# Kernel tuning notes

Measured on AMD Instinct MI355X. Metric: run time of the kernel, lower is better.

The kernel has to match this reference:

```python
import jax, jax.numpy as jnp
import numpy as np

NUM_HEADS = 8
D_MODEL = 512
D_K = D_MODEL // NUM_HEADS


def setup_inputs() -> dict:
    key = jax.random.key(0)
    ks = jax.random.split(key, 16)
    B, L, Dq = 4, 2048, 512
    s = 1.0 / np.sqrt(D_MODEL)
    inp = {
        "query": jax.random.normal(ks[0], (B, L, Dq), jnp.float32),
        "key": jax.random.normal(ks[1], (B, L, Dq), jnp.float32),
        "value": jax.random.normal(ks[2], (B, L, Dq), jnp.float32),
        "mask": jax.random.randint(ks[3], (B, L), 0, 2, jnp.int32),
        "Wq": jax.random.normal(ks[4], (Dq, D_MODEL), jnp.float32) * s,
        "bq": jax.random.normal(ks[5], (D_MODEL,), jnp.float32) * s,
        "Wk": jax.random.normal(ks[6], (Dq, D_MODEL), jnp.float32) * s,
        "bk": jax.random.normal(ks[7], (D_MODEL,), jnp.float32) * s,
        "Wv": jax.random.normal(ks[8], (Dq, D_MODEL), jnp.float32) * s,
        "bv": jax.random.normal(ks[9], (D_MODEL,), jnp.float32) * s,
        "Wo": jax.random.normal(ks[10], (D_MODEL, D_MODEL), jnp.float32) * s,
        "bo": jax.random.normal(ks[11], (D_MODEL,), jnp.float32) * s,
    }
    return inp


def _mha(query, key, value, mask, Wq, bq, Wk, bk, Wv, bv, Wo, bo):
    B, Q, _ = query.shape
    KV = key.shape[1]
    # projections, split into heads: (B, H, L, d_k)
    q = (query @ Wq + bq).reshape(B, Q, NUM_HEADS, D_K).transpose(0, 2, 1, 3)
    k = (key @ Wk + bk).reshape(B, KV, NUM_HEADS, D_K).transpose(0, 2, 1, 3)
    v = (value @ Wv + bv).reshape(B, KV, NUM_HEADS, D_K).transpose(0, 2, 1, 3)
    # full (B, H, Q, KV) score matrix, as in the original module
    scores = jnp.einsum("bhqd,bhkd->bhqk", q, k) / jnp.sqrt(jnp.asarray(D_K, q.dtype))
    m = (mask == 0)[:, None, None, :]  # (B,1,1,KV) broadcasting like unsqueeze(1)
    min_val = jnp.finfo(scores.dtype).min
    scores = jnp.where(m, min_val, scores)
    attn = jax.nn.softmax(scores, axis=-1)
    attn = jnp.where(m, 0.0, attn)
    xs = jnp.einsum("bhqk,bhkd->bhqd", attn, v)
    xs = xs.transpose(0, 2, 1, 3).reshape(B, Q, NUM_HEADS * D_K)
    return xs @ Wo + bo


def reference(query, key, value, mask, Wq, bq, Wk, bk, Wv, bv, Wo, bo):
    return _mha(query, key, value, mask, Wq, bq, Wk, bk, Wv, bv, Wo, bo)
```

## Files before the change

### kernel.cpp

```cpp
#include <hip/hip_runtime.h>
#include <math.h>

#define Bq 4
#define Lq 2048
#define NH 8
#define LDP6 36

typedef __attribute__((ext_vector_type(8))) __bf16 bf16x8;
typedef __attribute__((ext_vector_type(4))) float f32x4;
#define MFMA16(a,b,c) __builtin_amdgcn_mfma_f32_16x16x32_bf16(a,b,c,0,0,0)

__device__ __forceinline__ void async16(const void* g, void* l) {
    __builtin_amdgcn_global_load_lds(
        (const __attribute__((address_space(1))) unsigned int*)g,
        (__attribute__((address_space(3))) unsigned int*)l, 16, 0, 0);
}

__device__ __forceinline__ void splitbf(float x, ushort& h, ushort& l) {
    unsigned u = __float_as_uint(x);
    h = (ushort)(u >> 16);
    float hf = __uint_as_float(u & 0xffff0000u);
    l = (ushort)(__float_as_uint(x - hf) >> 16);
}
__device__ __forceinline__ ushort rnebf(float x) {
    unsigned u = __float_as_uint(x);
    return (ushort)((u + 0x7fffu + ((u >> 16) & 1u)) >> 16);
}

__global__ __launch_bounds__(256) void prep_kernel(
    const float* __restrict__ W0, const float* __restrict__ W1,
    const float* __restrict__ W2, const float* __restrict__ W3,
    ushort* __restrict__ WTh, ushort* __restrict__ WTl,
    const int* __restrict__ mask, int* __restrict__ idx, int* __restrict__ nvalid,
    const float* __restrict__ X0, const float* __restrict__ X1, const float* __restrict__ X2,
    ushort* __restrict__ Xr)
{
    const int tid = threadIdx.x;
    const int z = blockIdx.z;
    if (z < 3) {
        const float* X = (z == 0) ? X0 : (z == 1) ? X1 : X2;
        const size_t ebase = (size_t)blockIdx.x * 2048 + (size_t)tid * 8;
        float4 a = *(const float4*)(X + ebase);
        float4 bb = *(const float4*)(X + ebase + 4);
        float vv[8] = {a.x, a.y, a.z, a.w, bb.x, bb.y, bb.z, bb.w};
        ushort hs[8];
        #pragma unroll
        for (int j = 0; j < 8; ++j) hs[j] = rnebf(vv[j]);
        uint4 wh;
        wh.x = hs[0] | ((unsigned)hs[1] << 16); wh.y = hs[2] | ((unsigned)hs[3] << 16);
        wh.z = hs[4] | ((unsigned)hs[5] << 16); wh.w = hs[6] | ((unsigned)hs[7] << 16);
        *(uint4*)(Xr + (size_t)z * 8192 * 512 + ebase) = wh;
        return;
    }
    const int x = blockIdx.x;
    __shared__ float T[64][65];
    __shared__ int ss[256];
    if (x < 256) {
        const int m = x >> 6;
        const float* W = (m == 0) ? W0 : (m == 1) ? W1 : (m == 2) ? W2 : W3;
        const int k0 = ((x >> 3) & 7) * 64, n0 = (x & 7) * 64;
        #pragma unroll
        for (int i = 0; i < 4; ++i) {
            int u = tid + i * 256;
            int row = u >> 4, c4 = (u & 15) * 4;
            float4 v = *(const float4*)(W + (size_t)(k0 + row) * 512 + n0 + c4);
            T[row][c4 + 0] = v.x; T[row][c4 + 1] = v.y; T[row][c4 + 2] = v.z; T[row][c4 + 3] = v.w;
        }
        __syncthreads();
        #pragma unroll
        for (int i = 0; i < 2; ++i) {
            int u = tid + i * 256;
            int d = u >> 3, c8 = (u & 7) * 8;
            ushort hs[8], ls[8];
            #pragma unroll
            for (int j = 0; j < 8; ++j) splitbf(T[c8 + j][d], hs[j], ls[j]);
            uint4 wh, wl;
            wh.x = hs[0] | ((unsigned)hs[1] << 16); wh.y = hs[2] | ((unsigned)hs[3] << 16);
            wh.z = hs[4] | ((unsigned)hs[5] << 16); wh.w = hs[6] | ((unsigned)hs[7] << 16);
            wl.x = ls[0] | ((unsigned)ls[1] << 16); wl.y = ls[2] | ((unsigned)ls[3] << 16);
            wl.z = ls[4] | ((unsigned)ls[5] << 16); wl.w = ls[6] | ((unsigned)ls[7] << 16);
            size_t off = (size_t)(m * 512 + n0 + d) * 512 + k0 + c8;
            *(uint4*)(WTh + off) = wh;
            *(uint4*)(WTl + off) = wl;
        }
        return;
    }
    if (x < 260) {
        const int b = x - 256;
        int m[8], s = 0;
        #pragma unroll
        for (int j = 0; j < 8; ++j) { m[j] = (mask[b * 2048 + tid * 8 + j] != 0); s += m[j]; }
        int v = s;
        ss[tid] = v;
        __syncthreads();
        for (int off = 1; off < 256; off <<= 1) {
            int t_ = (tid >= off) ? ss[tid - off] : 0;
            __syncthreads();
            v += t_;
            ss[tid] = v;
            __syncthreads();
        }
        int pos = v - s;
        #pragma unroll
        for (int j = 0; j < 8; ++j) if (m[j]) idx[b * 2048 + pos++] = tid * 8 + j;
        int tot = ss[255];
        if (tid == 0) nvalid[b] = tot;
        for (int k = tot + tid; k < 2048; k += 256) idx[b * 2048 + k] = 0;
    }
}

union GS {
    struct {
        ushort A[2][4096];
        ushort B[2][4096];
    } s;
    ushort E[17408];
};

__global__ __launch_bounds__(256) void gemmqkv_kernel(
    const ushort* __restrict__ Xr,
    const int* __restrict__ idx, const int* __restrict__ nvalid,
    const ushort* __restrict__ BT,
    const float* __restrict__ b0, const float* __restrict__ b1, const float* __restrict__ b2,
    ushort* __restrict__ Qh, ushort* __restrict__ Khp, ushort* __restrict__ VhT)
{
    __shared__ __align__(16) GS gs;
    const int tid = threadIdx.x;
    const int wave = tid >> 6, lane = tid & 63;
    const int l15 = lane & 15, quad = lane >> 4;
    const int m0 = blockIdx.x * 128;
    const int yy = blockIdx.y;
    const int mi = yy >> 2, n0 = (yy & 3) * 128;
    const int nglob = mi * 512 + n0;
    const int b = m0 >> 11;

    if (mi >= 1) {
        int nv = nvalid[b];
        int nvpad = ((nv + 127) >> 7) << 7;
        if ((m0 & 2047) >= nvpad) return;
    }

    const float* bias = (mi == 0) ? b0 : (mi == 1) ? b1 : b2;
    const int wm = (wave & 1) * 64, wn = (wave >> 1) * 64;

    const ushort* AZ = Xr + (size_t)mi * 8192 * 512;
    const int arow = lane >> 2;
    const int acs = ((lane & 3) ^ ((arow >> 1) & 3)) * 8;
    const ushort* asrc[2]; int adst[2];
    #pragma unroll
    for (int j = 0; j < 2; ++j) {
        int rb = wave * 2 + j;
        int row = rb * 16 + arow;
        int grow = m0 + row, r = grow & 2047;
        int srow = (mi == 0) ? grow : (b * 2048 + idx[b * 2048 + r]);
        asrc[j] = AZ + (size_t)srow * 512 + acs;
        adst[j] = rb * 512 + lane * 8;
    }
    const int brow = lane >> 2;
    const int bcs = ((lane & 3) ^ (brow & 3)) * 8;
    const ushort* bsp[2]; int bdst[2];
    #pragma unroll
    for (int j = 0; j < 2; ++j) {
        int r2 = wave * 32 + j * 16 + brow;
        bsp[j] = BT + (size_t)(nglob + r2) * 512 + bcs;
        bdst[j] = wave * 1024 + j * 512 + lane * 8;
    }

    f32x4 acc[4][4];
    #pragma unroll
    for (int i = 0; i < 4; ++i)
        #pragma unroll
        for (int j = 0; j < 4; ++j) acc[i][j] = (f32x4){0.f, 0.f, 0.f, 0.f};

    #pragma unroll
    for (int j = 0; j < 2; ++j) {
        async16(asrc[j], &gs.s.A[0][adst[j]]);
        async16(bsp[j], &gs.s.B[0][bdst[j]]);
    }

    for (int t = 0; t < 16; ++t) {
        const int p = t & 1;
        __syncthreads();
        if (t < 15) {
            const int kn = (t + 1) * 32;
            #pragma unroll
            for (int j = 0; j < 2; ++j) {
                async16(asrc[j] + kn, &gs.s.A[1 - p][adst[j]]);
                async16(bsp[j] + kn, &gs.s.B[1 - p][bdst[j]]);
            }
        }
        bf16x8 af[4];
        #pragma unroll
        for (int ms = 0; ms < 4; ++ms) {
            int off = (wm + ms * 16 + l15) * 32 + (quad ^ ((l15 >> 1) & 3)) * 8;
            af[ms] = *(const bf16x8*)&gs.s.A[p][off];
        }
        #pragma unroll
        for (int ns = 0; ns < 4; ++ns) {
            int off = (wn + ns * 16 + l15) * 32 + (quad ^ (l15 & 3)) * 8;
            bf16x8 bf = *(const bf16x8*)&gs.s.B[p][off];
            #pragma unroll
            for (int ms = 0; ms < 4; ++ms)
                acc[ms][ns] = MFMA16(af[ms], bf, acc[ms][ns]);
        }
    }

    #pragma unroll
    for (int ns = 0; ns < 4; ++ns) {
        float bv = bias[n0 + wn + ns * 16 + l15];
        #pragma unroll
        for (int ms = 0; ms < 4; ++ms)
            #pragma unroll
            for (int r = 0; r < 4; ++r) acc[ms][ns][r] += bv;
    }

    const int h0 = n0 >> 6;
    const int rr0 = m0 & 2047;
    __syncthreads();
    #pragma unroll
    for (int ms = 0; ms < 4; ++ms) {
        #pragma unroll
        for (int ns = 0; ns < 4; ++ns) {
            int cl = wn + ns * 16 + l15;
            int rl = wm + ms * 16 + quad * 4;
            if (mi == 2) {
                ushort4 w4;
                #pragma unroll
                for (int r = 0; r < 4; ++r) ((ushort*)&w4)[r] = rnebf(acc[ms][ns][r]);
                *(ushort4*)&gs.E[cl * 136 + rl] = w4;
            } else {
                #pragma unroll
                for (int r = 0; r < 4; ++r) gs.E[(rl + r) * 136 + cl] = rnebf(acc[ms][ns][r]);
            }
        }
    }
    __syncthreads();
    if (mi == 2) {
        #pragma unroll
        for (int i = 0; i < 8; ++i) {
            int idx2 = tid + i * 256;
            int d = idx2 >> 4, rg = idx2 & 15;
            int head = d >> 6, dd = d & 63;
            uint4 u = *(const uint4*)&gs.E[d * 136 + rg * 8];
            *(uint4*)&VhT[((size_t)(b * 8 + h0 + head) * 64 + dd) * 2048 + rr0 + rg * 8] = u;
        }
    } else {
        ushort* dst = (mi == 0) ? Qh : Khp;
        #pragma unroll
        for (int i = 0; i < 8; ++i) {
            int idx2 = tid + i * 256;
            int row = idx2 >> 4, cg = idx2 & 15;
            int head = cg >> 3, c8 = (cg & 7) * 8;
            uint4 u = *(const uint4*)&gs.E[row * 136 + cg * 8];
            *(uint4*)&dst[((size_t)(b * 8 + h0 + head) * 2048 + rr0 + row) * 64 + c8] = u;
        }
    }
}

union GSO {
    struct {
        ushort A[2][4096];
        ushort Bh[2][4096];
        ushort Bl[2][4096];
    } s;
};

__global__ __launch_bounds__(256) void gemmo_kernel(
    const ushort* __restrict__ Ap,
    const ushort* __restrict__ BhT, const ushort* __restrict__ BlT,
    const float* __restrict__ bias, float* __restrict__ Cf)
{
    __shared__ __align__(16) GSO gs;
    const int tid = threadIdx.x;
    const int wave = tid >> 6, lane = tid & 63;
    const int l15 = lane & 15, quad = lane >> 4;
    const int m0 = blockIdx.x * 128;
    const int n0 = blockIdx.y * 128;
    const int wm = (wave & 1) * 64, wn = (wave >> 1) * 64;

    const int arow = lane >> 2;
    const int acs = ((lane & 3) ^ ((arow >> 1) & 3)) * 8;
    const ushort* asrc[2]; int adst[2];
    #pragma unroll
    for (int j = 0; j < 2; ++j) {
        int rb = wave * 2 + j;
        asrc[j] = Ap + (size_t)(m0 + rb * 16 + arow) * 512 + acs;
        adst[j] = rb * 512 + lane * 8;
    }
    const int brow = lane >> 2;
    const int bcs = ((lane & 3) ^ (brow & 3)) * 8;
    const ushort* bsh[2]; const ushort* bsl[2]; int bdst[2];
    #pragma unroll
    for (int j = 0; j < 2; ++j) {
        int r2 = wave * 32 + j * 16 + brow;
        bsh[j] = BhT + (size_t)(n0 + r2) * 512 + bcs;
        bsl[j] = BlT + (size_t)(n0 + r2) * 512 + bcs;
        bdst[j] = wave * 1024 + j * 512 + lane * 8;
    }

    f32x4 acc[4][4];
    #pragma unroll
    for (int i = 0; i < 4; ++i)
        #pragma unroll
        for (int j = 0; j < 4; ++j) acc[i][j] = (f32x4){0.f, 0.f, 0.f, 0.f};

    #pragma unroll
    for (int j = 0; j < 2; ++j) {
        async16(asrc[j], &gs.s.A[0][adst[j]]);
        async16(bsh[j], &gs.s.Bh[0][bdst[j]]);
        async16(bsl[j], &gs.s.Bl[0][bdst[j]]);
    }

    for (int t = 0; t < 16; ++t) {
        const int p = t & 1;
        __syncthreads();
        if (t < 15) {
            const int kn = (t + 1) * 32;
            #pragma unroll
            for (int j = 0; j < 2; ++j) {
                async16(asrc[j] + kn, &gs.s.A[1 - p][adst[j]]);
                async16(bsh[j] + kn, &gs.s.Bh[1 - p][bdst[j]]);
                async16(bsl[j] + kn, &gs.s.Bl[1 - p][bdst[j]]);
            }
        }
        bf16x8 af[4];
        #pragma unroll
        for (int ms = 0; ms < 4; ++ms) {
            int off = (wm + ms * 16 + l15) * 32 + (quad ^ ((l15 >> 1) & 3)) * 8;
            af[ms] = *(const bf16x8*)&gs.s.A[p][off];
        }
        #pragma unroll
        for (int ns = 0; ns < 4; ++ns) {
            int off = (wn + ns * 16 + l15) * 32 + (quad ^ (l15 & 3)) * 8;
            bf16x8 bfh = *(const bf16x8*)&gs.s.Bh[p][off];
            bf16x8 bfl = *(const bf16x8*)&gs.s.Bl[p][off];
            #pragma unroll
            for (int ms = 0; ms < 4; ++ms) {
                acc[ms][ns] = MFMA16(af[ms], bfl, acc[ms][ns]);
                acc[ms][ns] = MFMA16(af[ms], bfh, acc[ms][ns]);
            }
        }
    }

    #pragma unroll
    for (int ns = 0; ns < 4; ++ns) {
        float bv = bias[n0 + wn + ns * 16 + l15];
        #pragma unroll
        for (int ms = 0; ms < 4; ++ms) {
            int col = n0 + wn + ns * 16 + l15;
            #pragma unroll
            for (int r = 0; r < 4; ++r)
                Cf[(size_t)(m0 + wm + ms * 16 + quad * 4 + r) * 512 + col] = acc[ms][ns][r] + bv;
        }
    }
}

union SmemU {
    struct { ushort KVs[2][4][4096]; ushort Pp[8][64 * LDP6]; } p1;
    struct { float Obuf[4][64 * 68]; float Lbuf[4][64]; } p2;
};

__global__ __launch_bounds__(512, 2) void attn3_kernel(
    const ushort* __restrict__ Qh, const ushort* __restrict__ Kh,
    const ushort* __restrict__ VhT, const int* __restrict__ nvalid,
    ushort* __restrict__ XS)
{
    __shared__ SmemU smem;
    const int tid = threadIdx.x;
    const int wave = tid >> 6, lane = tid & 63;
    const int l15 = lane & 15, quad = lane >> 4;
    const int w4 = wave & 3, half = wave >> 2;
    const int bh = blockIdx.x, b = bh >> 3, h = bh & 7;
    const int q0 = blockIdx.y * 256;

    const int nv = nvalid[b];
    const int nt = (nv + 127) >> 7;
    const int kvofs = half * 64 * nt;

    bf16x8 qf[4][2];
    #pragma unroll
    for (int qs = 0; qs < 4; ++qs) {
        size_t qb = ((size_t)bh * 2048 + q0 + w4 * 64 + qs * 16 + l15) * 64 + quad * 8;
        qf[qs][0] = *(const bf16x8*)(Qh + qb);
        qf[qs][1] = *(const bf16x8*)(Qh + qb + 32);
    }

    const f32x4 z = {0.f, 0.f, 0.f, 0.f};
    f32x4 oacc[4][4];
    #pragma unroll
    for (int i = 0; i < 4; ++i)
        #pragma unroll
        for (int j = 0; j < 4; ++j) oacc[i][j] = z;
    float lacc[4] = {0.f, 0.f, 0.f, 0.f};

    const int rloc = lane >> 3, gsw = (lane & 7) ^ rloc;
    const ushort* sb[4]; size_t sstep[4]; int dofs[4];
    #pragma unroll
    for (int i = 0; i < 4; ++i) {
        int cc = wave * 4 + i;
        int hc = cc >> 4, r16 = cc & 15, pc = r16 >> 3, ic = r16 & 7;
        if (pc == 0) {
            sb[i] = Kh + ((size_t)(bh * 2048 + hc * 64 * nt + ic * 8 + rloc)) * 64 + gsw * 8;
            sstep[i] = (size_t)64 * 64;
        } else {
            sb[i] = VhT + ((size_t)(bh * 64 + ic * 8 + rloc)) * 2048 + hc * 64 * nt + gsw * 8;
            sstep[i] = 64;
        }
        dofs[i] = (hc * 2 + pc) * 4096 + ic * 512;
    }

    const int sw0 = (quad ^ (l15 & 7)) * 8;
    const float SCL = 0.18033688011112042f;

    if (nt > 0) {
        #pragma unroll
        for (int i = 0; i < 4; ++i)
            async16(sb[i], &smem.p1.KVs[0][0][0] + dofs[i]);
    }

    for (int t = 0; t < nt; ++t) {
        __syncthreads();
        if (t + 1 < nt) {
            #pragma unroll
            for (int i = 0; i < 4; ++i)
                async16(sb[i] + (size_t)(t + 1) * sstep[i], &smem.p1.KVs[(t + 1) & 1][0][0] + dofs[i]);
        }
        const int p = t & 1;
        const ushort* K0 = smem.p1.KVs[p][half * 2 + 0];
        const ushort* V0 = smem.p1.KVs[p][half * 2 + 1];
        ushort* Pw = smem.p1.Pp[wave];

        #pragma unroll
        for (int ks = 0; ks < 2; ++ks) {
            #pragma unroll
            for (int kt2 = 0; kt2 < 2; ++kt2) {
                const int kt = ks * 2 + kt2;
                const int kb = (kt * 16 + l15) * 64;
                bf16x8 ka0 = *(const bf16x8*)&K0[kb + sw0];
                bf16x8 ka1 = *(const bf16x8*)&K0[kb + (sw0 ^ 32)];
                const int kbase = kvofs + t * 64 + kt * 16 + quad * 4;
                float bias[4];
                #pragma unroll
                for (int r = 0; r < 4; ++r) bias[r] = (kbase + r < nv) ? 0.f : -1e38f;
                #pragma unroll
                for (int qs = 0; qs < 4; ++qs) {
                    f32x4 a = z;
                    a = MFMA16(ka0, qf[qs][0], a);
                    a = MFMA16(ka1, qf[qs][1], a);
                    float pv[4];
                    #pragma unroll
                    for (int r = 0; r < 4; ++r) {
                        float x = __builtin_fmaf(a[r], SCL, bias[r]);
                        float e; asm("v_exp_f32 %0, %1" : "=v"(e) : "v"(x));
                        lacc[qs] += e;
                        pv[r] = e;
                    }
                    unsigned u01, u23;
                    asm("v_cvt_pk_bf16_f32 %0, %1, %2" : "=v"(u01) : "v"(pv[0]), "v"(pv[1]));
                    asm("v_cvt_pk_bf16_f32 %0, %1, %2" : "=v"(u23) : "v"(pv[2]), "v"(pv[3]));
                    uint2 w2; w2.x = u01; w2.y = u23;
                    *(uint2*)&Pw[(qs * 16 + l15) * LDP6 + kt2 * 16 + quad * 4] = w2;
                }
            }
            const int svo = sw0 ^ (ks * 32);
            bf16x8 pf[4];
            #pragma unroll
            for (int qs = 0; qs < 4; ++qs)
                pf[qs] = *(const bf16x8*)&Pw[(qs * 16 + l15) * LDP6 + quad * 8];
            #pragma unroll
            for (int dsub = 0; dsub < 4; ++dsub) {
                const int vb = (dsub * 16 + l15) * 64;
                bf16x8 vh = *(const bf16x8*)&V0[vb + svo];
                #pragma unroll
                for (int qs = 0; qs < 4; ++qs)
                    oacc[qs][dsub] = MFMA16(vh, pf[qs], oacc[qs][dsub]);
            }
        }
    }

    float lv[4];
    #pragma unroll
    for (int qs = 0; qs < 4; ++qs) {
        float v = lacc[qs];
        v += __shfl_xor(v, 16);
        v += __shfl_xor(v, 32);
        lv[qs] = v;
    }

    __syncthreads();
    if (half == 1) {
        #pragma unroll
        for (int qs = 0; qs < 4; ++qs) {
            #pragma unroll
            for (int dsub = 0; dsub < 4; ++dsub) {
                float4 o4 = {oacc[qs][dsub][0], oacc[qs][dsub][1], oacc[qs][dsub][2], oacc[qs][dsub][3]};
                *(float4*)&smem.p2.Obuf[w4][(qs * 16 + l15) * 68 + dsub * 16 + quad * 4] = o4;
            }
            if (quad == 0) smem.p2.Lbuf[w4][qs * 16 + l15] = lv[qs];
        }
    }
    __syncthreads();
    if (half == 0) {
        #pragma unroll
        for (int qs = 0; qs < 4; ++qs) {
            float ltot = lv[qs] + smem.p2.Lbuf[w4][qs * 16 + l15];
            float inv = (ltot > 0.f) ? 1.f / ltot : 0.f;
            int row = q0 + w4 * 64 + qs * 16 + l15;
            ushort* rp = XS + ((size_t)(b * 2048 + row)) * 512 + h * 64;
            #pragma unroll
            for (int dsub = 0; dsub < 4; ++dsub) {
                float4 p4 = *(const float4*)&smem.p2.Obuf[w4][(qs * 16 + l15) * 68 + dsub * 16 + quad * 4];
                ushort4 hv;
                hv.x = rnebf((oacc[qs][dsub][0] + p4.x) * inv);
                hv.y = rnebf((oacc[qs][dsub][1] + p4.y) * inv);
                hv.z = rnebf((oacc[qs][dsub][2] + p4.z) * inv);
                hv.w = rnebf((oacc[qs][dsub][3] + p4.w) * inv);
                *(ushort4*)&rp[dsub * 16 + quad * 4] = hv;
            }
        }
    }
}

extern "C" void kernel_launch(void* const* d_in, const int* in_sizes, int n_in,
                              void* d_out, int out_size, void* d_ws, size_t ws_size,
                              hipStream_t stream) {
    const float* query = (const float*)d_in[0];
    const float* key   = (const float*)d_in[1];
    const float* value = (const float*)d_in[2];
    const int*   mask  = (const int*)d_in[3];
    const float* Wq = (const float*)d_in[4];
    const float* bq = (const float*)d_in[5];
    const float* Wk = (const float*)d_in[6];
    const float* bk = (const float*)d_in[7];
    const float* Wv = (const float*)d_in[8];
    const float* bv = (const float*)d_in[9];
    const float* Wo = (const float*)d_in[10];
    const float* bo = (const float*)d_in[11];

    char* w = (char*)d_ws;
    const size_t MB = (size_t)1 << 20;
    ushort* Qh  = (ushort*)(w + 0 * MB);
    ushort* XS  = (ushort*)(w + 8 * MB);
    ushort* Khp = (ushort*)(w + 16 * MB);
    ushort* VhT = (ushort*)(w + 24 * MB);
    ushort* WTh = (ushort*)(w + 32 * MB);
    ushort* WTl = (ushort*)(w + 34 * MB);
    int* idxbuf = (int*)(w + 36 * MB);
    int* nvbuf  = (int*)(w + 36 * MB + 65536);
    ushort* Xr  = (ushort*)(w + 40 * MB);

    prep_kernel<<<dim3(2048, 1, 4), 256, 0, stream>>>(
        Wq, Wk, Wv, Wo, WTh, WTl, mask, idxbuf, nvbuf, query, key, value, Xr);
    gemmqkv_kernel<<<dim3(64, 12), 256, 0, stream>>>(
        Xr, idxbuf, nvbuf, WTh, bq, bk, bv, Qh, Khp, VhT);
    attn3_kernel<<<dim3(32, 8), 512, 0, stream>>>(Qh, Khp, VhT, nvbuf, XS);
    gemmo_kernel<<<dim3(64, 4), 256, 0, stream>>>(
        XS, WTh + (size_t)1536 * 512, WTl + (size_t)1536 * 512, bo, (float*)d_out);
}
```

Before: 184.8 us.

## Halve attention query tile and read V directly from global memory

The attention kernel now handles 128 query rows per block instead of 256, which doubles the grid to 32x16 blocks and halves the per-wave accumulator and P-buffer footprint. V tiles are no longer staged through LDS with async loads. Each wave instead reads its V fragments straight from global (VhT) inside the PV loop, and only K is double-buffered in shared memory. This cuts LDS usage and register pressure to raise occupancy and parallelism. The cost is that K is loaded twice as often across blocks and V loads become uncoalesced global reads on the critical path.

```diff
diff --git a/kernel.cpp b/kernel.cpp
--- a/kernel.cpp
+++ b/kernel.cpp
@@ -356,8 +356,8 @@
 }
 
 union SmemU {
-    struct { ushort KVs[2][4][4096]; ushort Pp[8][64 * LDP6]; } p1;
-    struct { float Obuf[4][64 * 68]; float Lbuf[4][64]; } p2;
+    struct { ushort Ks[2][2][4096]; ushort Pp[8][32 * LDP6]; } p1;
+    struct { float Obuf[4][32 * 68]; float Lbuf[4][32]; } p2;
 };
 
 __global__ __launch_bounds__(512, 2) void attn3_kernel(
@@ -365,69 +365,63 @@
     const ushort* __restrict__ VhT, const int* __restrict__ nvalid,
     ushort* __restrict__ XS)
 {
-    __shared__ SmemU smem;
+    __shared__ __align__(16) SmemU smem;
     const int tid = threadIdx.x;
     const int wave = tid >> 6, lane = tid & 63;
     const int l15 = lane & 15, quad = lane >> 4;
     const int w4 = wave & 3, half = wave >> 2;
     const int bh = blockIdx.x, b = bh >> 3, h = bh & 7;
-    const int q0 = blockIdx.y * 256;
+    const int q0 = blockIdx.y * 128;
 
     const int nv = nvalid[b];
     const int nt = (nv + 127) >> 7;
     const int kvofs = half * 64 * nt;
 
-    bf16x8 qf[4][2];
-    #pragma unroll
-    for (int qs = 0; qs < 4; ++qs) {
-        size_t qb = ((size_t)bh * 2048 + q0 + w4 * 64 + qs * 16 + l15) * 64 + quad * 8;
+    bf16x8 qf[2][2];
+    #pragma unroll
+    for (int qs = 0; qs < 2; ++qs) {
+        size_t qb = ((size_t)bh * 2048 + q0 + w4 * 32 + qs * 16 + l15) * 64 + quad * 8;
         qf[qs][0] = *(const bf16x8*)(Qh + qb);
         qf[qs][1] = *(const bf16x8*)(Qh + qb + 32);
     }
 
     const f32x4 z = {0.f, 0.f, 0.f, 0.f};
-    f32x4 oacc[4][4];
-    #pragma unroll
-    for (int i = 0; i < 4; ++i)
+    f32x4 oacc[2][4];
+    #pragma unroll
+    for (int i = 0; i < 2; ++i)
         #pragma unroll
         for (int j = 0; j < 4; ++j) oacc[i][j] = z;
-    float lacc[4] = {0.f, 0.f, 0.f, 0.f};
+    float lacc[2] = {0.f, 0.f};
 
     const int rloc = lane >> 3, gsw = (lane & 7) ^ rloc;
-    const ushort* sb[4]; size_t sstep[4]; int dofs[4];
-    #pragma unroll
-    for (int i = 0; i < 4; ++i) {
-        int cc = wave * 4 + i;
-        int hc = cc >> 4, r16 = cc & 15, pc = r16 >> 3, ic = r16 & 7;
-        if (pc == 0) {
-            sb[i] = Kh + ((size_t)(bh * 2048 + hc * 64 * nt + ic * 8 + rloc)) * 64 + gsw * 8;
-            sstep[i] = (size_t)64 * 64;
-        } else {
-            sb[i] = VhT + ((size_t)(bh * 64 + ic * 8 + rloc)) * 2048 + hc * 64 * nt + gsw * 8;
-            sstep[i] = 64;
-        }
-        dofs[i] = (hc * 2 + pc) * 4096 + ic * 512;
-    }
+    const ushort* sb[2]; int dofs[2];
+    #pragma unroll
+    for (int i = 0; i < 2; ++i) {
+        int cc = wave * 2 + i;
+        int hc = cc >> 3, ic = cc & 7;
+        sb[i] = Kh + ((size_t)(bh * 2048 + hc * 64 * nt + ic * 8 + rloc)) * 64 + gsw * 8;
+        dofs[i] = hc * 4096 + ic * 512 + lane * 8;
+    }
+    const ushort* Vb = VhT + ((size_t)(bh * 64 + l15)) * 2048 + kvofs + quad * 8;
 
     const int sw0 = (quad ^ (l15 & 7)) * 8;
     const float SCL = 0.18033688011112042f;
 
     if (nt > 0) {
         #pragma unroll
-        for (int i = 0; i < 4; ++i)
-            async16(sb[i], &smem.p1.KVs[0][0][0] + dofs[i]);
+        for (int i = 0; i < 2; ++i)
+            async16(sb[i], &smem.p1.Ks[0][0][0] + dofs[i]);
     }
 
     for (int t = 0; t < nt; ++t) {
         __syncthreads();
         if (t + 1 < nt) {
             #pragma unroll
-            for (int i = 0; i < 4; ++i)
-                async16(sb[i] + (size_t)(t + 1) * sstep[i], &smem.p1.KVs[(t + 1) & 1][0][0] + dofs[i]);
+            for (int i = 0; i < 2; ++i)
+                async16(sb[i] + (size_t)(t + 1) * 64 * 64, &smem.p1.Ks[(t + 1) & 1][0][0] + dofs[i]);
         }
         const int p = t & 1;
-        const ushort* K0 = smem.p1.KVs[p][half * 2 + 0];
-        const ushort* V0 = smem.p1.KVs[p][half * 2 + 1];
+        const ushort* K0 = smem.p1.Ks[p][half];
         ushort* Pw = smem.p1.Pp[wave];
 
         #pragma unroll
@@ -443,7 +437,7 @@
                 #pragma unroll
                 for (int r = 0; r < 4; ++r) bias[r] = (kbase + r < nv) ? 0.f : -1e38f;
                 #pragma unroll
-                for (int qs = 0; qs < 4; ++qs) {
+                for (int qs = 0; qs < 2; ++qs) {
                     f32x4 a = z;
                     a = MFMA16(ka0, qf[qs][0], a);
                     a = MFMA16(ka1, qf[qs][1], a);
@@ -462,25 +456,23 @@
                     *(uint2*)&Pw[(qs * 16 + l15) * LDP6 + kt2 * 16 + quad * 4] = w2;
                 }
             }
-            const int svo = sw0 ^ (ks * 32);
-            bf16x8 pf[4];
-            #pragma unroll
-            for (int qs = 0; qs < 4; ++qs)
+            bf16x8 pf[2];
+            #pragma unroll
+            for (int qs = 0; qs < 2; ++qs)
                 pf[qs] = *(const bf16x8*)&Pw[(qs * 16 + l15) * LDP6 + quad * 8];
             #pragma unroll
             for (int dsub = 0; dsub < 4; ++dsub) {
-                const int vb = (dsub * 16 + l15) * 64;
-                bf16x8 vh = *(const bf16x8*)&V0[vb + svo];
+                bf16x8 vh = *(const bf16x8*)(Vb + (size_t)(dsub * 16) * 2048 + t * 64 + ks * 32);
                 #pragma unroll
-                for (int qs = 0; qs < 4; ++qs)
+                for (int qs = 0; qs < 2; ++qs)
                     oacc[qs][dsub] = MFMA16(vh, pf[qs], oacc[qs][dsub]);
             }
         }
     }
 
-    float lv[4];
-    #pragma unroll
-    for (int qs = 0; qs < 4; ++qs) {
+    float lv[2];
+    #pragma unroll
+    for (int qs = 0; qs < 2; ++qs) {
         float v = lacc[qs];
         v += __shfl_xor(v, 16);
         v += __shfl_xor(v, 32);
@@ -490,7 +482,7 @@
     __syncthreads();
     if (half == 1) {
         #pragma unroll
-        for (int qs = 0; qs < 4; ++qs) {
+        for (int qs = 0; qs < 2; ++qs) {
             #pragma unroll
             for (int dsub = 0; dsub < 4; ++dsub) {
                 float4 o4 = {oacc[qs][dsub][0], oacc[qs][dsub][1], oacc[qs][dsub][2], oacc[qs][dsub][3]};
@@ -502,10 +494,10 @@
     __syncthreads();
     if (half == 0) {
         #pragma unroll
-        for (int qs = 0; qs < 4; ++qs) {
+        for (int qs = 0; qs < 2; ++qs) {
             float ltot = lv[qs] + smem.p2.Lbuf[w4][qs * 16 + l15];
             float inv = (ltot > 0.f) ? 1.f / ltot : 0.f;
-            int row = q0 + w4 * 64 + qs * 16 + l15;
+            int row = q0 + w4 * 32 + qs * 16 + l15;
             ushort* rp = XS + ((size_t)(b * 2048 + row)) * 512 + h * 64;
             #pragma unroll
             for (int dsub = 0; dsub < 4; ++dsub) {
@@ -553,7 +545,7 @@
         Wq, Wk, Wv, Wo, WTh, WTl, mask, idxbuf, nvbuf, query, key, value, Xr);
     gemmqkv_kernel<<<dim3(64, 12), 256, 0, stream>>>(
         Xr, idxbuf, nvbuf, WTh, bq, bk, bv, Qh, Khp, VhT);
-    attn3_kernel<<<dim3(32, 8), 512, 0, stream>>>(Qh, Khp, VhT, nvbuf, XS);
+    attn3_kernel<<<dim3(32, 16), 512, 0, stream>>>(Qh, Khp, VhT, nvbuf, XS);
     gemmo_kernel<<<dim3(64, 4), 256, 0, stream>>>(
         XS, WTh + (size_t)1536 * 512, WTl + (size_t)1536 * 512, bo, (float*)d_out);
 }
```

Result: slower. 190.3 us (+3.0%).

## Fuse fp32-to-bf16 input conversion into QKV GEMM A-tile loading

Applied to the files above, without the earlier changes.

Drops the separate pass in the prep kernel that converted query/key/value to bf16 and wrote them to a workspace buffer. The QKV GEMM now streams fp32 activations straight into LDS with async loads and converts them to bf16 with packed convert instructions when building MFMA fragments. This removes a full read-write pass over the three inputs, and the compacted key/value rows are gathered directly from fp32. In exchange the A tile doubles in LDS size and global A traffic inside the GEMM doubles. Rounding also moves to the hardware convert instruction instead of the manual RNE code.

```diff
diff --git a/kernel.cpp b/kernel.cpp
--- a/kernel.cpp
+++ b/kernel.cpp
@@ -31,27 +31,9 @@
     const float* __restrict__ W0, const float* __restrict__ W1,
     const float* __restrict__ W2, const float* __restrict__ W3,
     ushort* __restrict__ WTh, ushort* __restrict__ WTl,
-    const int* __restrict__ mask, int* __restrict__ idx, int* __restrict__ nvalid,
-    const float* __restrict__ X0, const float* __restrict__ X1, const float* __restrict__ X2,
-    ushort* __restrict__ Xr)
+    const int* __restrict__ mask, int* __restrict__ idx, int* __restrict__ nvalid)
 {
     const int tid = threadIdx.x;
-    const int z = blockIdx.z;
-    if (z < 3) {
-        const float* X = (z == 0) ? X0 : (z == 1) ? X1 : X2;
-        const size_t ebase = (size_t)blockIdx.x * 2048 + (size_t)tid * 8;
-        float4 a = *(const float4*)(X + ebase);
-        float4 bb = *(const float4*)(X + ebase + 4);
-        float vv[8] = {a.x, a.y, a.z, a.w, bb.x, bb.y, bb.z, bb.w};
-        ushort hs[8];
-        #pragma unroll
-        for (int j = 0; j < 8; ++j) hs[j] = rnebf(vv[j]);
-        uint4 wh;
-        wh.x = hs[0] | ((unsigned)hs[1] << 16); wh.y = hs[2] | ((unsigned)hs[3] << 16);
-        wh.z = hs[4] | ((unsigned)hs[5] << 16); wh.w = hs[6] | ((unsigned)hs[7] << 16);
-        *(uint4*)(Xr + (size_t)z * 8192 * 512 + ebase) = wh;
-        return;
-    }
     const int x = blockIdx.x;
     __shared__ float T[64][65];
     __shared__ int ss[256];
@@ -111,14 +93,14 @@
 
 union GS {
     struct {
-        ushort A[2][4096];
+        float  A[2][4096];
         ushort B[2][4096];
     } s;
-    ushort E[17408];
+    ushort E[24576];
 };
 
 __global__ __launch_bounds__(256) void gemmqkv_kernel(
-    const ushort* __restrict__ Xr,
+    const float* __restrict__ Xq, const float* __restrict__ Xk, const float* __restrict__ Xv,
     const int* __restrict__ idx, const int* __restrict__ nvalid,
     const ushort* __restrict__ BT,
     const float* __restrict__ b0, const float* __restrict__ b1, const float* __restrict__ b2,
@@ -140,21 +122,20 @@
         if ((m0 & 2047) >= nvpad) return;
     }
 
+    const float* X = (mi == 0) ? Xq : (mi == 1) ? Xk : Xv;
     const float* bias = (mi == 0) ? b0 : (mi == 1) ? b1 : b2;
     const int wm = (wave & 1) * 64, wn = (wave >> 1) * 64;
 
-    const ushort* AZ = Xr + (size_t)mi * 8192 * 512;
-    const int arow = lane >> 2;
-    const int acs = ((lane & 3) ^ ((arow >> 1) & 3)) * 8;
-    const ushort* asrc[2]; int adst[2];
-    #pragma unroll
-    for (int j = 0; j < 2; ++j) {
-        int rb = wave * 2 + j;
-        int row = rb * 16 + arow;
+    const int arow8 = lane >> 3;
+    const int asg = (lane & 7) ^ (arow8 & 7);
+    const float* asrcf[4]; int adstf[4];
+    #pragma unroll
+    for (int i = 0; i < 4; ++i) {
+        int row = wave * 32 + i * 8 + arow8;
         int grow = m0 + row, r = grow & 2047;
         int srow = (mi == 0) ? grow : (b * 2048 + idx[b * 2048 + r]);
-        asrc[j] = AZ + (size_t)srow * 512 + acs;
-        adst[j] = rb * 512 + lane * 8;
+        asrcf[i] = X + (size_t)srow * 512 + asg * 4;
+        adstf[i] = ((wave * 4 + i) * 64 + lane) * 4;
     }
     const int brow = lane >> 2;
     const int bcs = ((lane & 3) ^ (brow & 3)) * 8;
@@ -173,10 +154,9 @@
         for (int j = 0; j < 4; ++j) acc[i][j] = (f32x4){0.f, 0.f, 0.f, 0.f};
 
     #pragma unroll
-    for (int j = 0; j < 2; ++j) {
-        async16(asrc[j], &gs.s.A[0][adst[j]]);
-        async16(bsp[j], &gs.s.B[0][bdst[j]]);
-    }
+    for (int i = 0; i < 4; ++i) async16(asrcf[i], &gs.s.A[0][adstf[i]]);
+    #pragma unroll
+    for (int j = 0; j < 2; ++j) async16(bsp[j], &gs.s.B[0][bdst[j]]);
 
     for (int t = 0; t < 16; ++t) {
         const int p = t & 1;
@@ -184,16 +164,26 @@
         if (t < 15) {
             const int kn = (t + 1) * 32;
             #pragma unroll
-            for (int j = 0; j < 2; ++j) {
-                async16(asrc[j] + kn, &gs.s.A[1 - p][adst[j]]);
-                async16(bsp[j] + kn, &gs.s.B[1 - p][bdst[j]]);
-            }
+            for (int i = 0; i < 4; ++i) async16(asrcf[i] + kn, &gs.s.A[1 - p][adstf[i]]);
+            #pragma unroll
+            for (int j = 0; j < 2; ++j) async16(bsp[j] + kn * 1, &gs.s.B[1 - p][bdst[j]]);
         }
         bf16x8 af[4];
         #pragma unroll
         for (int ms = 0; ms < 4; ++ms) {
-            int off = (wm + ms * 16 + l15) * 32 + (quad ^ ((l15 >> 1) & 3)) * 8;
-            af[ms] = *(const bf16x8*)&gs.s.A[p][off];
+            int R = wm + ms * 16 + l15;
+            int s = l15 & 7;
+            const float4* rowp = (const float4*)&gs.s.A[p][R * 32];
+            float4 fa = rowp[(2 * quad) ^ s];
+            float4 fb = rowp[(2 * quad + 1) ^ s];
+            unsigned c0, c1, c2, c3;
+            asm("v_cvt_pk_bf16_f32 %0, %1, %2" : "=v"(c0) : "v"(fa.x), "v"(fa.y));
+            asm("v_cvt_pk_bf16_f32 %0, %1, %2" : "=v"(c1) : "v"(fa.z), "v"(fa.w));
+            asm("v_cvt_pk_bf16_f32 %0, %1, %2" : "=v"(c2) : "v"(fb.x), "v"(fb.y));
+            asm("v_cvt_pk_bf16_f32 %0, %1, %2" : "=v"(c3) : "v"(fb.z), "v"(fb.w));
+            union { uint4 u; bf16x8 v; } cv;
+            cv.u.x = c0; cv.u.y = c1; cv.u.z = c2; cv.u.w = c3;
+            af[ms] = cv.v;
         }
         #pragma unroll
         for (int ns = 0; ns < 4; ++ns) {
@@ -547,12 +537,11 @@
     ushort* WTl = (ushort*)(w + 34 * MB);
     int* idxbuf = (int*)(w + 36 * MB);
     int* nvbuf  = (int*)(w + 36 * MB + 65536);
-    ushort* Xr  = (ushort*)(w + 40 * MB);
-
-    prep_kernel<<<dim3(2048, 1, 4), 256, 0, stream>>>(
-        Wq, Wk, Wv, Wo, WTh, WTl, mask, idxbuf, nvbuf, query, key, value, Xr);
+
+    prep_kernel<<<dim3(260), 256, 0, stream>>>(
+        Wq, Wk, Wv, Wo, WTh, WTl, mask, idxbuf, nvbuf);
     gemmqkv_kernel<<<dim3(64, 12), 256, 0, stream>>>(
-        Xr, idxbuf, nvbuf, WTh, bq, bk, bv, Qh, Khp, VhT);
+        query, key, value, idxbuf, nvbuf, WTh, bq, bk, bv, Qh, Khp, VhT);
     attn3_kernel<<<dim3(32, 8), 512, 0, stream>>>(Qh, Khp, VhT, nvbuf, XS);
     gemmo_kernel<<<dim3(64, 4), 256, 0, stream>>>(
         XS, WTh + (size_t)1536 * 512, WTl + (size_t)1536 * 512, bo, (float*)d_out);
```

Result: slower. 193.9 us (+5.0%).
